# Kernel tuning notes

Measured on AMD Instinct MI355X. Metric: run time of the kernel, lower is better.

## Reference

```python
import jax, jax.numpy as jnp
import numpy as np

DT = 0.001          # time step
P = 2               # geomloss p -> cost = ||x-y||^2 / 2, eps = blur**p
BLUR = 0.01
SCALING = 0.5       # eps annealing ratio per step is SCALING**P
SPARSE = 1          # sparse_sampling
N_STEPS = 24        # fixed annealing+refinement iteration count (jit-static)


def setup_inputs() -> dict:
    key = jax.random.key(0)
    k1, k2 = jax.random.split(key)
    B, S, NT, NR = 2, 4, 256, 64
    syn_data = jax.random.normal(k1, (B, S, NT, NR), jnp.float32)
    obs_data = jax.random.normal(k2, (B, S, NT, NR), jnp.float32)
    return {"syn_data": syn_data, "obs_data": obs_data}


def _softmin(eps, C, h):
    # h: [m] = log-weights + potential/eps ; C: [n, m]
    return -eps * jax.nn.logsumexp(h[None, :] - C / eps, axis=1)


def _pairwise_cost(a, b):
    # geomloss p=2 cost: squared euclidean distance / 2
    return 0.5 * jnp.sum((a[:, None, :] - b[None, :, :]) ** 2, axis=-1)


def _sinkhorn_divergence(x, y):
    # x, y: [n, 2] point clouds with uniform weights 1/n.
    # Debiased Sinkhorn divergence S = OT_eps(x,y) - 0.5 OT(x,x) - 0.5 OT(y,y)
    # computed via log-domain iterations with epsilon annealing from
    # diameter**p down to blur**p (ratio scaling**p), as in geomloss.
    n = x.shape[0]
    la = jnp.full((n,), -np.log(n), x.dtype)  # log uniform weights
    Cxy = _pairwise_cost(x, y)
    Cyx = Cxy.T
    Cxx = _pairwise_cost(x, x)
    Cyy = _pairwise_cost(y, y)

    xy = jnp.concatenate([x, y], axis=0)
    diameter = jnp.max(jnp.max(xy, axis=0) - jnp.min(xy, axis=0))
    eps0 = diameter ** P
    eps_min = jnp.asarray(BLUR ** P, x.dtype)
    ratio = SCALING ** P
    eps_list = jnp.maximum(eps0 * ratio ** jnp.arange(N_STEPS, dtype=x.dtype), eps_min)

    zeros = jnp.zeros((n,), x.dtype)

    def step(carry, eps):
        f, g, px, py = carry
        f_new = _softmin(eps, Cxy, la + g / eps)
        g_new = _softmin(eps, Cyx, la + f / eps)
        # symmetric (debiasing) potentials use damped fixed-point updates
        px_new = 0.5 * (px + _softmin(eps, Cxx, la + px / eps))
        py_new = 0.5 * (py + _softmin(eps, Cyy, la + py / eps))
        return (f_new, g_new, px_new, py_new), None

    (f, g, px, py), _ = jax.lax.scan(step, (zeros, zeros, zeros, zeros), eps_list)
    w = jnp.exp(la)  # uniform 1/n
    return jnp.sum(w * (f - px)) + jnp.sum(w * (g - py))


def reference(syn_data, obs_data):
    B, S, NT, NR = syn_data.shape
    # trace mask: drop receiver only if BOTH obs and syn traces are all-zero
    mask1 = jnp.sum(jnp.abs(obs_data), axis=2) == 0  # [B,S,NR]
    mask2 = jnp.sum(jnp.abs(syn_data), axis=2) == 0
    mask = ~(mask1 & mask2)

    t = jnp.arange(NT, dtype=syn_data.dtype)[::SPARSE] * DT  # [NTs]
    obs_tr = jnp.swapaxes(obs_data[:, :, ::SPARSE, :], 2, 3)  # [B,S,NR,NTs]
    syn_tr = jnp.swapaxes(syn_data[:, :, ::SPARSE, :], 2, 3)
    tb = jnp.broadcast_to(t, obs_tr.shape)
    obs_pts = jnp.stack([tb, obs_tr], axis=-1)  # [B,S,NR,NTs,2]
    syn_pts = jnp.stack([tb, syn_tr], axis=-1)

    nts = obs_pts.shape[3]
    flat_obs = obs_pts.reshape(B * S * NR, nts, 2)
    flat_syn = syn_pts.reshape(B * S * NR, nts, 2)
    div = jax.vmap(_sinkhorn_divergence)(flat_obs, flat_syn)  # [B*S*NR]
    div = div.reshape(B, S, NR)
    return jnp.sum(jnp.where(mask, div, jnp.zeros_like(div)), axis=(1, 2))  # [B]
```

## Files before the change

### kernel.cpp

```cpp
#include <hip/hip_runtime.h>


constexpr int   N       = 256;
constexpr int   NPROB   = 512;
constexpr int   NRDIM   = 64;
constexpr float DT_F    = 0.001f;
constexpr float EPS_MIN = 1e-4f;
constexpr int   NSTEPS  = 24;
constexpr float LOG2E   = 1.4426950408889634f;
constexpr float LN2     = 0.6931471805599453f;
constexpr int   NT      = 1024;
constexpr int   CPQ     = 64;

extern "C" __global__ void __launch_bounds__(NT, 8)
sinkhorn_div_kernel(const float* __restrict__ syn,
                    const float* __restrict__ obs,
                    float* __restrict__ divs)
{
    const int p   = blockIdx.x;
    const int r   = p & (NRDIM - 1);
    const int bs  = p >> 6;
    const int tid = threadIdx.x;
    const int row = tid & (N - 1);
    const int q   = tid >> 8;

    __shared__ float4 ya[N];
    __shared__ float4 xa[N];
    __shared__ float4 msh[NT];
    __shared__ float4 ssh[NT];
    __shared__ float  redA[64];

    const size_t base = (size_t)bs * N * NRDIM + r;
    const float xi = obs[base + (size_t)row * NRDIM];
    const float yi = syn[base + (size_t)row * NRDIM];

    float hi = fmaxf(xi, yi), lo = fminf(xi, yi);
    float ax = fabsf(xi),     ay = fabsf(yi);
    #pragma unroll
    for (int off = 32; off > 0; off >>= 1) {
        hi  = fmaxf(hi, __shfl_down(hi, off, 64));
        lo  = fminf(lo, __shfl_down(lo, off, 64));
        ax += __shfl_down(ax, off, 64);
        ay += __shfl_down(ay, off, 64);
    }
    const int wave = tid >> 6;
    if ((tid & 63) == 0) {
        redA[wave * 4 + 0] = hi;  redA[wave * 4 + 1] = lo;
        redA[wave * 4 + 2] = ax;  redA[wave * 4 + 3] = ay;
    }
    __syncthreads();
    float vmax = -3.4e38f, vmin = 3.4e38f, sax = 0.0f, say = 0.0f;
    #pragma unroll
    for (int w = 0; w < 16; ++w) {
        vmax = fmaxf(vmax, redA[w * 4 + 0]);
        vmin = fminf(vmin, redA[w * 4 + 1]);
        sax += redA[w * 4 + 2];
        say += redA[w * 4 + 3];
    }

    const float tspread  = 255.0f * DT_F;
    const float diameter = fmaxf(tspread, vmax - vmin);
    float eps_raw = diameter * diameter;

    const float ti    = (float)row * DT_F;
    const float selfx = 0.5f * (ti * ti + xi * xi);
    const float selfy = 0.5f * (ti * ti + yi * yi);

    float f = 0.0f, g = 0.0f, px = 0.0f, py = 0.0f;

    const int j0 = q * CPQ;

#define EXP2(x) __builtin_amdgcn_exp2f(x)

#define CHUNK(ARR) \
        { \
            const float4 Q0 = ARR[jb + 0]; \
            const float4 Q1 = ARR[jb + 1]; \
            const float4 Q2 = ARR[jb + 2]; \
            const float4 Q3 = ARR[jb + 3]; \
            const float4 Q4 = ARR[jb + 4]; \
            const float4 Q5 = ARR[jb + 5]; \
            const float4 Q6 = ARR[jb + 6]; \
            const float4 Q7 = ARR[jb + 7]; \
            const float b0 = fmaf(ti, Q0.w, fmaf(C1, Q0.z, Q0.x)); \
            const float c0 = fmaf(ti, Q0.w, fmaf(C2, Q0.z, Q0.y)); \
            const float b1 = fmaf(ti, Q1.w, fmaf(C1, Q1.z, Q1.x)); \
            const float c1 = fmaf(ti, Q1.w, fmaf(C2, Q1.z, Q1.y)); \
            const float b2 = fmaf(ti, Q2.w, fmaf(C1, Q2.z, Q2.x)); \
            const float c2 = fmaf(ti, Q2.w, fmaf(C2, Q2.z, Q2.y)); \
            const float b3 = fmaf(ti, Q3.w, fmaf(C1, Q3.z, Q3.x)); \
            const float c3 = fmaf(ti, Q3.w, fmaf(C2, Q3.z, Q3.y)); \
            const float b4 = fmaf(ti, Q4.w, fmaf(C1, Q4.z, Q4.x)); \
            const float c4 = fmaf(ti, Q4.w, fmaf(C2, Q4.z, Q4.y)); \
            const float b5 = fmaf(ti, Q5.w, fmaf(C1, Q5.z, Q5.x)); \
            const float c5 = fmaf(ti, Q5.w, fmaf(C2, Q5.z, Q5.y)); \
            const float b6 = fmaf(ti, Q6.w, fmaf(C1, Q6.z, Q6.x)); \
            const float c6 = fmaf(ti, Q6.w, fmaf(C2, Q6.z, Q6.y)); \
            const float b7 = fmaf(ti, Q7.w, fmaf(C1, Q7.z, Q7.x)); \
            const float c7 = fmaf(ti, Q7.w, fmaf(C2, Q7.z, Q7.y)); \
             \
            const float bt0 = fmaxf(fmaxf(b0, b1), b2); \
            const float bt1 = fmaxf(fmaxf(b3, b4), b5); \
            const float bt2 = fmaxf(fmaxf(b6, b7), m0); \
            const float M0  = ceilf(fmaxf(fmaxf(bt0, bt1), bt2)); \
            const float ct0 = fmaxf(fmaxf(c0, c1), c2); \
            const float ct1 = fmaxf(fmaxf(c3, c4), c5); \
            const float ct2 = fmaxf(fmaxf(c6, c7), m1); \
            const float M1  = ceilf(fmaxf(fmaxf(ct0, ct1), ct2)); \
            const float t0 = \
                ((EXP2(b0 - M0) + EXP2(b1 - M0)) + (EXP2(b2 - M0) + EXP2(b3 - M0))) + \
                ((EXP2(b4 - M0) + EXP2(b5 - M0)) + (EXP2(b6 - M0) + EXP2(b7 - M0))); \
            const float t1 = \
                ((EXP2(c0 - M1) + EXP2(c1 - M1)) + (EXP2(c2 - M1) + EXP2(c3 - M1))) + \
                ((EXP2(c4 - M1) + EXP2(c5 - M1)) + (EXP2(c6 - M1) + EXP2(c7 - M1))); \
            s0 = ldexpf(s0, (int)(m0 - M0)) + t0;  m0 = M0; \
            s1 = ldexpf(s1, (int)(m1 - M1)) + t1;  m1 = M1; \
        }

    for (int step = 0; step < NSTEPS; ++step) {
        const float eps = fmaxf(eps_raw, EPS_MIN);
        const float inv = LOG2E / eps;

        if (q == 0) {
            const float la2 = -8.0f;
            const float Hxy = fmaf(g  - selfy, inv, la2);
            const float Hyy = fmaf(py - selfy, inv, la2);
            const float Hyx = fmaf(f  - selfx, inv, la2);
            const float Hxx = fmaf(px - selfx, inv, la2);
            const float tji = ti * inv;
            ya[row] = make_float4(Hxy, Hyy, yi * inv, tji);
            xa[row] = make_float4(Hyx, Hxx, xi * inv, tji);
        }
        __syncthreads();

        {
            float m0 = -1e9f, m1 = -1e9f, s0 = 0.0f, s1 = 0.0f;
            const float C1 = xi, C2 = yi;
            #pragma unroll
            for (int cc = 0; cc < CPQ; cc += 8) {
                const int jb = j0 + cc;
                CHUNK(ya)
            }
            msh[tid] = make_float4(m0, m1, s0, s1);
        }

        {
            float m0 = -1e9f, m1 = -1e9f, s0 = 0.0f, s1 = 0.0f;
            const float C1 = yi, C2 = xi;
            #pragma unroll
            for (int cc = 0; cc < CPQ; cc += 8) {
                const int jb = j0 + cc;
                CHUNK(xa)
            }
            ssh[tid] = make_float4(m0, m1, s0, s1);
        }
        __syncthreads();

        if (q == 0) {
            const float4 A0 = msh[row];
            const float4 A1 = msh[row + 256];
            const float4 A2 = msh[row + 512];
            const float4 A3 = msh[row + 768];
            const float4 B0 = ssh[row];
            const float4 B1 = ssh[row + 256];
            const float4 B2 = ssh[row + 512];
            const float4 B3 = ssh[row + 768];

            const float Mxy = fmaxf(fmaxf(A0.x, A1.x), fmaxf(A2.x, A3.x));
            const float Myy = fmaxf(fmaxf(A0.y, A1.y), fmaxf(A2.y, A3.y));
            const float Myx = fmaxf(fmaxf(B0.x, B1.x), fmaxf(B2.x, B3.x));
            const float Mxx = fmaxf(fmaxf(B0.y, B1.y), fmaxf(B2.y, B3.y));

            const float Sxy = (ldexpf(A0.z, (int)(A0.x - Mxy)) + ldexpf(A1.z, (int)(A1.x - Mxy)))
                            + (ldexpf(A2.z, (int)(A2.x - Mxy)) + ldexpf(A3.z, (int)(A3.x - Mxy)));
            const float Syy = (ldexpf(A0.w, (int)(A0.y - Myy)) + ldexpf(A1.w, (int)(A1.y - Myy)))
                            + (ldexpf(A2.w, (int)(A2.y - Myy)) + ldexpf(A3.w, (int)(A3.y - Myy)));
            const float Syx = (ldexpf(B0.z, (int)(B0.x - Myx)) + ldexpf(B1.z, (int)(B1.x - Myx)))
                            + (ldexpf(B2.z, (int)(B2.x - Myx)) + ldexpf(B3.z, (int)(B3.x - Myx)));
            const float Sxx = (ldexpf(B0.w, (int)(B0.y - Mxx)) + ldexpf(B1.w, (int)(B1.y - Mxx)))
                            + (ldexpf(B2.w, (int)(B2.y - Mxx)) + ldexpf(B3.w, (int)(B3.y - Mxx)));

            const float el2 = eps * LN2;
            const float fn  = selfx - el2 * (Mxy + __builtin_amdgcn_logf(Sxy));
            const float gn  = selfy - el2 * (Myx + __builtin_amdgcn_logf(Syx));
            const float pxn = 0.5f * (px + (selfx - el2 * (Mxx + __builtin_amdgcn_logf(Sxx))));
            const float pyn = 0.5f * (py + (selfy - el2 * (Myy + __builtin_amdgcn_logf(Syy))));
            f = fn; g = gn; px = pxn; py = pyn;
        }

        eps_raw *= 0.25f;
    }
#undef CHUNK
#undef EXP2

    float contrib = (q == 0) ? ((f - px) + (g - py)) : 0.0f;
    #pragma unroll
    for (int off = 32; off > 0; off >>= 1)
        contrib += __shfl_down(contrib, off, 64);
    __syncthreads();
    if ((tid & 63) == 0) redA[wave] = contrib;
    __syncthreads();
    if (tid == 0) {
        float total = 0.0f;
        #pragma unroll
        for (int w = 0; w < 16; ++w) total += redA[w];
        total *= (1.0f / (float)N);
        const bool masked_out = (sax == 0.0f) && (say == 0.0f);
        divs[p] = masked_out ? 0.0f : total;
    }
}

extern "C" __global__ void __launch_bounds__(256)
reduce_out_kernel(const float* __restrict__ divs, float* __restrict__ out)
{
    const int b   = blockIdx.x;
    const int tid = threadIdx.x;
    __shared__ float red[4];
    float v = divs[b * 256 + tid];
    #pragma unroll
    for (int off = 32; off > 0; off >>= 1)
        v += __shfl_down(v, off, 64);
    if ((tid & 63) == 0) red[tid >> 6] = v;
    __syncthreads();
    if (tid == 0) out[b] = red[0] + red[1] + red[2] + red[3];
}

extern "C" void kernel_launch(void* const* d_in, const int* in_sizes, int n_in,
                              void* d_out, int out_size, void* d_ws, size_t ws_size,
                              hipStream_t stream) {
    const float* syn = (const float*)d_in[0];
    const float* obs = (const float*)d_in[1];
    float* divs = (float*)d_ws;

    sinkhorn_div_kernel<<<NPROB, NT, 0, stream>>>(syn, obs, divs);
    reduce_out_kernel<<<2, 256, 0, stream>>>(divs, (float*)d_out);
}
```

Baseline: 599.3 us.

## Split potential updates across two thread groups and software-pipeline LDS loads

The serial per-step work is now split between two thread quarters: q==0 owns the x-side potentials (f, px) and q==1 owns the y-side ones (g, py). Each group writes only its own shared array and finalizes only its own logsumexp pair, which halves the serial tail that other waves wait on at each barrier. The inner chunk loop is also restructured into 4-element groups with double-buffered register prefetch of the next group's float4 LDS loads, so load latency overlaps with the exp work. The smaller chunks mean more frequent running-max rescaling (ldexp) and higher register pressure from the prefetch buffers.

```diff
diff --git a/kernel.cpp b/kernel.cpp
--- a/kernel.cpp
+++ b/kernel.cpp
@@ -11,6 +11,7 @@
 constexpr float LN2     = 0.6931471805599453f;
 constexpr int   NT      = 1024;
 constexpr int   CPQ     = 64;
+constexpr int   NHALF   = CPQ / 4;
 
 extern "C" __global__ void __launch_bounds__(NT, 8)
 sinkhorn_div_kernel(const float* __restrict__ syn,
@@ -65,6 +66,7 @@
     const float ti    = (float)row * DT_F;
     const float selfx = 0.5f * (ti * ti + xi * xi);
     const float selfy = 0.5f * (ti * ti + yi * yi);
+    const float la2   = -8.0f;
 
     float f = 0.0f, g = 0.0f, px = 0.0f, py = 0.0f;
 
@@ -72,49 +74,30 @@
 
 #define EXP2(x) __builtin_amdgcn_exp2f(x)
 
-#define CHUNK(ARR) \
+#define PRE(ARR, P0, P1, P2, P3, H) \
+            P0 = ARR[j0 + (H) * 4 + 0]; \
+            P1 = ARR[j0 + (H) * 4 + 1]; \
+            P2 = ARR[j0 + (H) * 4 + 2]; \
+            P3 = ARR[j0 + (H) * 4 + 3];
+
+#define COMP(P0, P1, P2, P3) \
         { \
-            const float4 Q0 = ARR[jb + 0]; \
-            const float4 Q1 = ARR[jb + 1]; \
-            const float4 Q2 = ARR[jb + 2]; \
-            const float4 Q3 = ARR[jb + 3]; \
-            const float4 Q4 = ARR[jb + 4]; \
-            const float4 Q5 = ARR[jb + 5]; \
-            const float4 Q6 = ARR[jb + 6]; \
-            const float4 Q7 = ARR[jb + 7]; \
-            const float b0 = fmaf(ti, Q0.w, fmaf(C1, Q0.z, Q0.x)); \
-            const float c0 = fmaf(ti, Q0.w, fmaf(C2, Q0.z, Q0.y)); \
-            const float b1 = fmaf(ti, Q1.w, fmaf(C1, Q1.z, Q1.x)); \
-            const float c1 = fmaf(ti, Q1.w, fmaf(C2, Q1.z, Q1.y)); \
-            const float b2 = fmaf(ti, Q2.w, fmaf(C1, Q2.z, Q2.x)); \
-            const float c2 = fmaf(ti, Q2.w, fmaf(C2, Q2.z, Q2.y)); \
-            const float b3 = fmaf(ti, Q3.w, fmaf(C1, Q3.z, Q3.x)); \
-            const float c3 = fmaf(ti, Q3.w, fmaf(C2, Q3.z, Q3.y)); \
-            const float b4 = fmaf(ti, Q4.w, fmaf(C1, Q4.z, Q4.x)); \
-            const float c4 = fmaf(ti, Q4.w, fmaf(C2, Q4.z, Q4.y)); \
-            const float b5 = fmaf(ti, Q5.w, fmaf(C1, Q5.z, Q5.x)); \
-            const float c5 = fmaf(ti, Q5.w, fmaf(C2, Q5.z, Q5.y)); \
-            const float b6 = fmaf(ti, Q6.w, fmaf(C1, Q6.z, Q6.x)); \
-            const float c6 = fmaf(ti, Q6.w, fmaf(C2, Q6.z, Q6.y)); \
-            const float b7 = fmaf(ti, Q7.w, fmaf(C1, Q7.z, Q7.x)); \
-            const float c7 = fmaf(ti, Q7.w, fmaf(C2, Q7.z, Q7.y)); \
-             \
-            const float bt0 = fmaxf(fmaxf(b0, b1), b2); \
-            const float bt1 = fmaxf(fmaxf(b3, b4), b5); \
-            const float bt2 = fmaxf(fmaxf(b6, b7), m0); \
-            const float M0  = ceilf(fmaxf(fmaxf(bt0, bt1), bt2)); \
-            const float ct0 = fmaxf(fmaxf(c0, c1), c2); \
-            const float ct1 = fmaxf(fmaxf(c3, c4), c5); \
-            const float ct2 = fmaxf(fmaxf(c6, c7), m1); \
-            const float M1  = ceilf(fmaxf(fmaxf(ct0, ct1), ct2)); \
-            const float t0 = \
-                ((EXP2(b0 - M0) + EXP2(b1 - M0)) + (EXP2(b2 - M0) + EXP2(b3 - M0))) + \
-                ((EXP2(b4 - M0) + EXP2(b5 - M0)) + (EXP2(b6 - M0) + EXP2(b7 - M0))); \
-            const float t1 = \
-                ((EXP2(c0 - M1) + EXP2(c1 - M1)) + (EXP2(c2 - M1) + EXP2(c3 - M1))) + \
-                ((EXP2(c4 - M1) + EXP2(c5 - M1)) + (EXP2(c6 - M1) + EXP2(c7 - M1))); \
-            s0 = ldexpf(s0, (int)(m0 - M0)) + t0;  m0 = M0; \
-            s1 = ldexpf(s1, (int)(m1 - M1)) + t1;  m1 = M1; \
+            const float b0_ = fmaf(ti, P0.w, fmaf(C1, P0.z, P0.x)); \
+            const float c0_ = fmaf(ti, P0.w, fmaf(C2, P0.z, P0.y)); \
+            const float b1_ = fmaf(ti, P1.w, fmaf(C1, P1.z, P1.x)); \
+            const float c1_ = fmaf(ti, P1.w, fmaf(C2, P1.z, P1.y)); \
+            const float b2_ = fmaf(ti, P2.w, fmaf(C1, P2.z, P2.x)); \
+            const float c2_ = fmaf(ti, P2.w, fmaf(C2, P2.z, P2.y)); \
+            const float b3_ = fmaf(ti, P3.w, fmaf(C1, P3.z, P3.x)); \
+            const float c3_ = fmaf(ti, P3.w, fmaf(C2, P3.z, P3.y)); \
+            const float Mb = fmaxf(m0, ceilf(fmaxf(fmaxf(b0_, b1_), fmaxf(b2_, b3_)))); \
+            const float Mc = fmaxf(m1, ceilf(fmaxf(fmaxf(c0_, c1_), fmaxf(c2_, c3_)))); \
+            const float tb = (EXP2(b0_ - Mb) + EXP2(b1_ - Mb)) \
+                           + (EXP2(b2_ - Mb) + EXP2(b3_ - Mb)); \
+            const float tc = (EXP2(c0_ - Mc) + EXP2(c1_ - Mc)) \
+                           + (EXP2(c2_ - Mc) + EXP2(c3_ - Mc)); \
+            s0 = ldexpf(s0, (int)(m0 - Mb)) + tb;  m0 = Mb; \
+            s1 = ldexpf(s1, (int)(m1 - Mc)) + tc;  m1 = Mc; \
         }
 
     for (int step = 0; step < NSTEPS; ++step) {
@@ -122,24 +105,27 @@
         const float inv = LOG2E / eps;
 
         if (q == 0) {
-            const float la2 = -8.0f;
+            const float Hyx = fmaf(f  - selfx, inv, la2);
+            const float Hxx = fmaf(px - selfx, inv, la2);
+            xa[row] = make_float4(Hyx, Hxx, xi * inv, ti * inv);
+        } else if (q == 1) {
             const float Hxy = fmaf(g  - selfy, inv, la2);
             const float Hyy = fmaf(py - selfy, inv, la2);
-            const float Hyx = fmaf(f  - selfx, inv, la2);
-            const float Hxx = fmaf(px - selfx, inv, la2);
-            const float tji = ti * inv;
-            ya[row] = make_float4(Hxy, Hyy, yi * inv, tji);
-            xa[row] = make_float4(Hyx, Hxx, xi * inv, tji);
+            ya[row] = make_float4(Hxy, Hyy, yi * inv, ti * inv);
         }
         __syncthreads();
 
         {
             float m0 = -1e9f, m1 = -1e9f, s0 = 0.0f, s1 = 0.0f;
             const float C1 = xi, C2 = yi;
+            float4 A0, A1, A2, A3, D0, D1, D2, D3;
+            PRE(ya, A0, A1, A2, A3, 0)
             #pragma unroll
-            for (int cc = 0; cc < CPQ; cc += 8) {
-                const int jb = j0 + cc;
-                CHUNK(ya)
+            for (int h = 0; h < NHALF; h += 2) {
+                PRE(ya, D0, D1, D2, D3, h + 1)
+                COMP(A0, A1, A2, A3)
+                if (h + 2 < NHALF) { PRE(ya, A0, A1, A2, A3, h + 2) }
+                COMP(D0, D1, D2, D3)
             }
             msh[tid] = make_float4(m0, m1, s0, s1);
         }
@@ -147,16 +133,20 @@
         {
             float m0 = -1e9f, m1 = -1e9f, s0 = 0.0f, s1 = 0.0f;
             const float C1 = yi, C2 = xi;
+            float4 A0, A1, A2, A3, D0, D1, D2, D3;
+            PRE(xa, A0, A1, A2, A3, 0)
             #pragma unroll
-            for (int cc = 0; cc < CPQ; cc += 8) {
-                const int jb = j0 + cc;
-                CHUNK(xa)
+            for (int h = 0; h < NHALF; h += 2) {
+                PRE(xa, D0, D1, D2, D3, h + 1)
+                COMP(A0, A1, A2, A3)
+                if (h + 2 < NHALF) { PRE(xa, A0, A1, A2, A3, h + 2) }
+                COMP(D0, D1, D2, D3)
             }
             ssh[tid] = make_float4(m0, m1, s0, s1);
         }
         __syncthreads();
 
-        if (q == 0) {
+        if (q <= 1) {
             const float4 A0 = msh[row];
             const float4 A1 = msh[row + 256];
             const float4 A2 = msh[row + 512];
@@ -165,35 +155,37 @@
             const float4 B1 = ssh[row + 256];
             const float4 B2 = ssh[row + 512];
             const float4 B3 = ssh[row + 768];
-
-            const float Mxy = fmaxf(fmaxf(A0.x, A1.x), fmaxf(A2.x, A3.x));
-            const float Myy = fmaxf(fmaxf(A0.y, A1.y), fmaxf(A2.y, A3.y));
-            const float Myx = fmaxf(fmaxf(B0.x, B1.x), fmaxf(B2.x, B3.x));
-            const float Mxx = fmaxf(fmaxf(B0.y, B1.y), fmaxf(B2.y, B3.y));
-
-            const float Sxy = (ldexpf(A0.z, (int)(A0.x - Mxy)) + ldexpf(A1.z, (int)(A1.x - Mxy)))
-                            + (ldexpf(A2.z, (int)(A2.x - Mxy)) + ldexpf(A3.z, (int)(A3.x - Mxy)));
-            const float Syy = (ldexpf(A0.w, (int)(A0.y - Myy)) + ldexpf(A1.w, (int)(A1.y - Myy)))
-                            + (ldexpf(A2.w, (int)(A2.y - Myy)) + ldexpf(A3.w, (int)(A3.y - Myy)));
-            const float Syx = (ldexpf(B0.z, (int)(B0.x - Myx)) + ldexpf(B1.z, (int)(B1.x - Myx)))
-                            + (ldexpf(B2.z, (int)(B2.x - Myx)) + ldexpf(B3.z, (int)(B3.x - Myx)));
-            const float Sxx = (ldexpf(B0.w, (int)(B0.y - Mxx)) + ldexpf(B1.w, (int)(B1.y - Mxx)))
-                            + (ldexpf(B2.w, (int)(B2.y - Mxx)) + ldexpf(B3.w, (int)(B3.y - Mxx)));
-
             const float el2 = eps * LN2;
-            const float fn  = selfx - el2 * (Mxy + __builtin_amdgcn_logf(Sxy));
-            const float gn  = selfy - el2 * (Myx + __builtin_amdgcn_logf(Syx));
-            const float pxn = 0.5f * (px + (selfx - el2 * (Mxx + __builtin_amdgcn_logf(Sxx))));
-            const float pyn = 0.5f * (py + (selfy - el2 * (Myy + __builtin_amdgcn_logf(Syy))));
-            f = fn; g = gn; px = pxn; py = pyn;
+            if (q == 0) {
+                const float Mxy = fmaxf(fmaxf(A0.x, A1.x), fmaxf(A2.x, A3.x));
+                const float Sxy = (ldexpf(A0.z, (int)(A0.x - Mxy)) + ldexpf(A1.z, (int)(A1.x - Mxy)))
+                                + (ldexpf(A2.z, (int)(A2.x - Mxy)) + ldexpf(A3.z, (int)(A3.x - Mxy)));
+                const float Mxx = fmaxf(fmaxf(B0.y, B1.y), fmaxf(B2.y, B3.y));
+                const float Sxx = (ldexpf(B0.w, (int)(B0.y - Mxx)) + ldexpf(B1.w, (int)(B1.y - Mxx)))
+                                + (ldexpf(B2.w, (int)(B2.y - Mxx)) + ldexpf(B3.w, (int)(B3.y - Mxx)));
+                f  = selfx - el2 * (Mxy + __builtin_amdgcn_logf(Sxy));
+                px = 0.5f * (px + (selfx - el2 * (Mxx + __builtin_amdgcn_logf(Sxx))));
+            } else {
+                const float Myx = fmaxf(fmaxf(B0.x, B1.x), fmaxf(B2.x, B3.x));
+                const float Syx = (ldexpf(B0.z, (int)(B0.x - Myx)) + ldexpf(B1.z, (int)(B1.x - Myx)))
+                                + (ldexpf(B2.z, (int)(B2.x - Myx)) + ldexpf(B3.z, (int)(B3.x - Myx)));
+                const float Myy = fmaxf(fmaxf(A0.y, A1.y), fmaxf(A2.y, A3.y));
+                const float Syy = (ldexpf(A0.w, (int)(A0.y - Myy)) + ldexpf(A1.w, (int)(A1.y - Myy)))
+                                + (ldexpf(A2.w, (int)(A2.y - Myy)) + ldexpf(A3.w, (int)(A3.y - Myy)));
+                g  = selfy - el2 * (Myx + __builtin_amdgcn_logf(Syx));
+                py = 0.5f * (py + (selfy - el2 * (Myy + __builtin_amdgcn_logf(Syy))));
+            }
         }
 
         eps_raw *= 0.25f;
     }
-#undef CHUNK
+#undef COMP
+#undef PRE
 #undef EXP2
 
-    float contrib = (q == 0) ? ((f - px) + (g - py)) : 0.0f;
+    float contrib = 0.0f;
+    if (q == 0)      contrib = f - px;
+    else if (q == 1) contrib = g - py;
     #pragma unroll
     for (int off = 32; off > 0; off >>= 1)
         contrib += __shfl_down(contrib, off, 64);
```

Result: slower. 685.2 us (+14.3%).
